# Kernel tuning notes

Hardware: AMD Instinct MI355X
Metric: run time of the kernel (lower is better)

## Reference

```python
import jax, jax.numpy as jnp
import numpy as np

GAMMA = 10.0          # entropy_regularizer_weight
N_ITERS = 10          # optimization_steps
EPS = np.float32(7.0 / 3 - 4.0 / 3 - 1.0)  # matches tf.constant(7/3-4/3-1, float32)

B, W, H, D = 128, 28, 28, 512
S = 128               # support_size


def setup_inputs() -> dict:
    key = jax.random.key(0)
    k1, k2 = jax.random.split(key)
    features = jax.random.normal(k1, (B, W, H, D), dtype=jnp.float32)
    # GlorotUniform-like init for the target support (learned codebook)
    limit = np.sqrt(6.0 / (S + D)).astype(np.float32)
    target_support = jax.random.uniform(k2, (S, D), dtype=jnp.float32,
                                        minval=-limit, maxval=limit)
    return {"features": features, "target_support": target_support}


def _l2norm(x):
    return x / jnp.sqrt(jnp.sum(x * x, axis=-1, keepdims=True))


def reference(features, target_support):
    b, w, h, d = features.shape
    s = target_support.shape[0]
    n = w * h  # num_feats

    t = _l2norm(target_support)                 # (S, D)
    f = _l2norm(features).reshape(b, n, d)      # (B, N, D)

    # pairwise squared L2 distance between normalized vectors: 2 - 2*cos
    c = 2.0 - 2.0 * jnp.einsum('sd,bnd->bsn', t, f)  # (B, S, N)

    K = jnp.exp(-GAMMA * c)                     # (B, S, N)
    q = jnp.full((1, 1, n), 1.0 / n, dtype=jnp.float32)  # marginal over feats
    p = jnp.full((1, 1, s), 1.0 / s, dtype=jnp.float32)  # marginal over support

    u = jnp.ones((b, 1, s), dtype=jnp.float32)
    Kt = jnp.swapaxes(K, 1, 2)                  # (B, N, S)
    for _ in range(N_ITERS):
        v = q / (jnp.matmul(u, K) + EPS)        # (B, 1, N)
        u = p / (jnp.matmul(v, Kt) + EPS)       # (B, 1, S)
    v = q / (jnp.matmul(u, K) + EPS)

    # transport plan Pi = u^T * K * v  -> (B, S, N)
    Pi = jnp.swapaxes(u, 1, 2) * K * v
    return Pi
```

## Files before the change

kernel.cpp:

```cpp
#include <hip/hip_runtime.h>
#include <hip/hip_fp16.h>

#define EPS_C   2.2204460492503131e-16f
#define NS      128
#define ND      512
#define NN      784
#define NB      128
#define BSN     (NS*NN)
#define QM      (1.0f/784.0f)
#define LOG2E20 28.853900817779268f

typedef __attribute__((ext_vector_type(8))) short bf16x8;
typedef __attribute__((ext_vector_type(4))) float f32x4;

static __device__ __forceinline__ ushort f2bf(float x) {
    uint u = __float_as_uint(x);
    uint r = (u + 0x7FFFu + ((u >> 16) & 1u)) >> 16;
    return (ushort)r;
}
static __device__ __forceinline__ float bf2f(ushort h) {
    return __uint_as_float(((uint)h) << 16);
}

__global__ __launch_bounds__(128)
void tnorm_kernel(const float* __restrict__ t,
                  ushort* __restrict__ tnh, ushort* __restrict__ tnl) {
    int s = blockIdx.x, tid = threadIdx.x;
    float4 x = ((const float4*)(t + s * ND))[tid];
    float ss = x.x*x.x + x.y*x.y + x.z*x.z + x.w*x.w;
#pragma unroll
    for (int off = 1; off < 64; off <<= 1) ss += __shfl_xor(ss, off);
    __shared__ float red[2];
    if ((tid & 63) == 0) red[tid >> 6] = ss;
    __syncthreads();
    float rs = 1.0f / sqrtf(red[0] + red[1]);
    float y[4] = {x.x*rs, x.y*rs, x.z*rs, x.w*rs};
    ushort h[4], l[4];
#pragma unroll
    for (int k = 0; k < 4; k++) {
        h[k] = f2bf(y[k]);
        l[k] = f2bf(y[k] - bf2f(h[k]));
    }
    *(ushort4*)(tnh + s * ND + tid * 4) = make_ushort4(h[0], h[1], h[2], h[3]);
    *(ushort4*)(tnl + s * ND + tid * 4) = make_ushort4(l[0], l[1], l[2], l[3]);
}

#define LDK 40

__global__ void __launch_bounds__(256)
__attribute__((amdgpu_waves_per_eu(2, 2)))
gemm_k_kernel(const ushort* __restrict__ Ahi, const ushort* __restrict__ Alo,
              const float* __restrict__ f, uint* __restrict__ Kp) {
    __shared__ ushort Ash[2][NS * LDK];
    __shared__ ushort Bsh[2][NS * LDK];
    __shared__ float  ssq_sh[128];

    const int tid  = threadIdx.x;
    const int lane = tid & 63;
    const int wid  = tid >> 6;
    const int wm   = wid & 1;
    const int wn   = wid >> 1;
    const int j0   = blockIdx.x * 128;

    const int arow  = tid & 127;
    const int ahalf = tid >> 7;
    const int brow  = tid >> 3;
    const int bcol4 = (tid & 7) * 4;

    const ushort* Asrc = (ahalf ? Alo : Ahi) + (size_t)arow * ND;
    const float* bPtr[4];
#pragma unroll
    for (int p = 0; p < 4; p++)
        bPtr[p] = f + (size_t)(j0 + p * 32 + brow) * ND + bcol4;

    f32x4 acc[4][4];
#pragma unroll
    for (int i = 0; i < 4; i++)
#pragma unroll
        for (int j = 0; j < 4; j++) acc[i][j] = (f32x4){0.f, 0.f, 0.f, 0.f};
    float ssqp[4] = {0.f, 0.f, 0.f, 0.f};

    const int mrow = lane & 15;
    const int koff = (lane >> 4) * 8;

    uint4 aReg[4];
    float4 bReg[4];
    {
        const uint4* ap = (const uint4*)Asrc;
        aReg[0] = ap[0]; aReg[1] = ap[1]; aReg[2] = ap[2]; aReg[3] = ap[3];
#pragma unroll
        for (int p = 0; p < 4; p++) bReg[p] = *(const float4*)bPtr[p];
    }

    for (int d0 = 0; d0 < ND; d0 += 32) {
        {
            ushort* dst = &Ash[ahalf][arow * LDK];
            *(uint4*)(dst)      = aReg[0];
            *(uint4*)(dst + 8)  = aReg[1];
            *(uint4*)(dst + 16) = aReg[2];
            *(uint4*)(dst + 24) = aReg[3];
        }
#pragma unroll
        for (int p = 0; p < 4; p++) {
            float4 v = bReg[p];
            ssqp[p] += v.x*v.x + v.y*v.y + v.z*v.z + v.w*v.w;
            ushort h0 = f2bf(v.x), h1 = f2bf(v.y), h2 = f2bf(v.z), h3 = f2bf(v.w);
            ushort l0 = f2bf(v.x - bf2f(h0)), l1 = f2bf(v.y - bf2f(h1));
            ushort l2 = f2bf(v.z - bf2f(h2)), l3 = f2bf(v.w - bf2f(h3));
            int c = p * 32 + brow;
            *(uint2*)&Bsh[0][c * LDK + bcol4] =
                make_uint2((uint)h0 | ((uint)h1 << 16), (uint)h2 | ((uint)h3 << 16));
            *(uint2*)&Bsh[1][c * LDK + bcol4] =
                make_uint2((uint)l0 | ((uint)l1 << 16), (uint)l2 | ((uint)l3 << 16));
        }
        __syncthreads();
        if (d0 + 32 < ND) {
            const uint4* ap = (const uint4*)(Asrc + d0 + 32);
            aReg[0] = ap[0]; aReg[1] = ap[1]; aReg[2] = ap[2]; aReg[3] = ap[3];
#pragma unroll
            for (int p = 0; p < 4; p++)
                bReg[p] = *(const float4*)(bPtr[p] + d0 + 32);
        }
        bf16x8 ah[4], bb[4];
#pragma unroll
        for (int i = 0; i < 4; i++)
            ah[i] = *(const bf16x8*)&Ash[0][(wm*64 + i*16 + mrow) * LDK + koff];
#pragma unroll
        for (int j = 0; j < 4; j++)
            bb[j] = *(const bf16x8*)&Bsh[0][(wn*64 + j*16 + mrow) * LDK + koff];
#pragma unroll
        for (int i = 0; i < 4; i++)
#pragma unroll
            for (int j = 0; j < 4; j++)
                acc[i][j] = __builtin_amdgcn_mfma_f32_16x16x32_bf16(ah[i], bb[j], acc[i][j], 0, 0, 0);
        {
            bf16x8 al[4];
#pragma unroll
            for (int i = 0; i < 4; i++)
                al[i] = *(const bf16x8*)&Ash[1][(wm*64 + i*16 + mrow) * LDK + koff];
#pragma unroll
            for (int i = 0; i < 4; i++)
#pragma unroll
                for (int j = 0; j < 4; j++)
                    acc[i][j] = __builtin_amdgcn_mfma_f32_16x16x32_bf16(al[i], bb[j], acc[i][j], 0, 0, 0);
        }
#pragma unroll
        for (int j = 0; j < 4; j++)
            bb[j] = *(const bf16x8*)&Bsh[1][(wn*64 + j*16 + mrow) * LDK + koff];
#pragma unroll
        for (int i = 0; i < 4; i++)
#pragma unroll
            for (int j = 0; j < 4; j++)
                acc[i][j] = __builtin_amdgcn_mfma_f32_16x16x32_bf16(ah[i], bb[j], acc[i][j], 0, 0, 0);
        __syncthreads();
    }

#pragma unroll
    for (int p = 0; p < 4; p++) {
#pragma unroll
        for (int off = 1; off < 8; off <<= 1) ssqp[p] += __shfl_xor(ssqp[p], off);
    }
    if ((tid & 7) == 0) {
#pragma unroll
        for (int p = 0; p < 4; p++) ssq_sh[p * 32 + (tid >> 3)] = ssqp[p];
    }
    __syncthreads();

    const int quad4 = (lane >> 4) << 2;
#pragma unroll
    for (int jt = 0; jt < 4; jt++) {
        int cloc = wn * 64 + jt * 16 + mrow;
        float rq = rsqrtf(ssq_sh[cloc]) * LOG2E20;
        int jg = j0 + cloc;
        int b2 = jg / NN;
        int nn = jg - b2 * NN;
        int jj = nn >> 6, l = nn & 63;
#pragma unroll
        for (int i = 0; i < 4; i++) {
            int s0 = wm * 64 + i * 16 + quad4;
            float k0 = exp2f(acc[i][jt][0] * rq);
            float k1 = exp2f(acc[i][jt][1] * rq);
            float k2v = exp2f(acc[i][jt][2] * rq);
            float k3 = exp2f(acc[i][jt][3] * rq);
            __half2 lo = __halves2half2(__float2half(k0), __float2half(k1));
            __half2 hi = __halves2half2(__float2half(k2v), __float2half(k3));
            size_t dw = (((size_t)(b2 * 16 + (s0 >> 3)) * 13 + jj) * 64 + l) * 4
                        + ((s0 & 7) >> 1);
            *(uint2*)(Kp + dw) = make_uint2(__builtin_bit_cast(uint, lo),
                                            __builtin_bit_cast(uint, hi));
        }
    }
}

#define VSCALE 64.0f
#define PM64   (VSCALE/128.0f)
#define EPS64  (EPS_C*VSCALE)

__global__ void __launch_bounds__(1024)
__attribute__((amdgpu_waves_per_eu(4, 4)))
sinkhorn_kernel(const uint* __restrict__ Kp, float* __restrict__ Pi) {
    __shared__ float slab[16 * NN];
    __shared__ float v_sh[NN];
    const int b    = blockIdx.x;
    const int tid  = threadIdx.x;
    const int lane = tid & 63;
    const int w    = tid >> 6;
    float* Pib = Pi + (size_t)b * BSN;

    const uint4* kbase = (const uint4*)Kp + (size_t)(b * 16 + w) * 13 * 64 + lane;
    __half2 k2[13][4];
#pragma unroll
    for (int j = 0; j < 13; j++) {
        uint4 t = kbase[j * 64];
        k2[j][0] = __builtin_bit_cast(__half2, t.x);
        k2[j][1] = __builtin_bit_cast(__half2, t.y);
        k2[j][2] = __builtin_bit_cast(__half2, t.z);
        k2[j][3] = __builtin_bit_cast(__half2, t.w);
    }
    if (lane >= 16) {
#pragma unroll
        for (int rp = 0; rp < 4; rp++) k2[12][rp] = __halves2half2(__half(0.f), __half(0.f));
    }

    __half2 u2[4];
    float uf[8];
#pragma unroll
    for (int rp = 0; rp < 4; rp++) u2[rp] = __halves2half2(__half(1.f), __half(1.f));
#pragma unroll
    for (int r = 0; r < 8; r++) uf[r] = 1.f;

    float* myrow = &slab[w * NN];

    for (int it = 0; it <= 10; ++it) {
#pragma unroll
        for (int j = 0; j < 13; j++) {
            int n = lane + (j << 6);
            float pa = 0.f;
#pragma unroll
            for (int rp = 0; rp < 4; rp++)
                pa = __builtin_amdgcn_fdot2(k2[j][rp], u2[rp], pa, false);
            if (n < NN) myrow[n] = pa;
        }
        __syncthreads();
        if (tid < NN) {
            float s0 = 0.f, s1 = 0.f, s2 = 0.f, s3 = 0.f;
#pragma unroll
            for (int w2 = 0; w2 < 16; w2 += 4) {
                s0 += slab[(w2 + 0) * NN + tid];
                s1 += slab[(w2 + 1) * NN + tid];
                s2 += slab[(w2 + 2) * NN + tid];
                s3 += slab[(w2 + 3) * NN + tid];
            }
            v_sh[tid] = QM / (((s0 + s1) + (s2 + s3)) + EPS_C);
        }
        __syncthreads();
        if (it == 10) break;
        __half2 acc2[4];
#pragma unroll
        for (int rp = 0; rp < 4; rp++) acc2[rp] = __halves2half2(__half(0.f), __half(0.f));
#pragma unroll
        for (int j = 0; j < 13; j++) {
            int n = lane + (j << 6);
            int ni = (n < NN) ? n : 0;
            float vv = v_sh[ni] * VSCALE;
            __half vh = __float2half(vv);
            __half2 vh2 = __halves2half2(vh, vh);
#pragma unroll
            for (int rp = 0; rp < 4; rp++)
                acc2[rp] = __hfma2(vh2, k2[j][rp], acc2[rp]);
        }
#pragma unroll
        for (int rp = 0; rp < 4; rp++) {
#pragma unroll
            for (int off = 1; off < 64; off <<= 1) {
                int y = __shfl_xor(__builtin_bit_cast(int, acc2[rp]), off);
                acc2[rp] = __hadd2(acc2[rp], __builtin_bit_cast(__half2, y));
            }
            float2 af = __half22float2(acc2[rp]);
            uf[2*rp]     = PM64 / (af.x + EPS64);
            uf[2*rp + 1] = PM64 / (af.y + EPS64);
            u2[rp] = __halves2half2(__float2half(uf[2*rp]), __float2half(uf[2*rp+1]));
        }
    }

#pragma unroll
    for (int j = 0; j < 13; j++) {
        int n = lane + (j << 6);
        if (n < NN) {
            float vv = v_sh[n];
#pragma unroll
            for (int rp = 0; rp < 4; rp++) {
                float2 kk = __half22float2(k2[j][rp]);
                Pib[(size_t)(8*w + 2*rp    ) * NN + n] = uf[2*rp]     * kk.x * vv;
                Pib[(size_t)(8*w + 2*rp + 1) * NN + n] = uf[2*rp + 1] * kk.y * vv;
            }
        }
    }
}

extern "C" void kernel_launch(void* const* d_in, const int* in_sizes, int n_in,
                              void* d_out, int out_size, void* d_ws, size_t ws_size,
                              hipStream_t stream) {
    const float* feat = (const float*)d_in[0];
    const float* tsup = (const float*)d_in[1];
    float* out = (float*)d_out;

    ushort* tnh = (ushort*)d_ws;
    ushort* tnl = tnh + NS * ND;
    uint*   Kp  = (uint*)(tnl + NS * ND);

    tnorm_kernel<<<NS, 128, 0, stream>>>(tsup, tnh, tnl);
    gemm_k_kernel<<<(NB * NN) / 128, 256, 0, stream>>>(tnh, tnl, feat, Kp);
    sinkhorn_kernel<<<NB, 1024, 0, stream>>>(Kp, out);
}
```

Baseline: 366.5 us.

## Load A fragments directly from global, use packed bf16 convert, relax occupancy

The GEMM kernel no longer stages the normalized support (hi/lo bf16 split) through shared memory. Each wave now loads its MFMA A fragments straight from global memory (L2-resident, 128x512), which removes half the LDS traffic and footprint. The hi/lo bf16 split of the features now uses the hardware v_cvt_pk_bf16_f32 instruction instead of manual rounding. waves_per_eu is widened to allow more occupancy. The catch is that A loads are no longer prefetched a tile ahead, so global latency may be exposed just before the MFMAs. Redundant A reads across the wn waves also rely on cache.

```diff
diff --git a/kernel.cpp b/kernel.cpp
--- a/kernel.cpp
+++ b/kernel.cpp
@@ -21,6 +21,11 @@
 static __device__ __forceinline__ float bf2f(ushort h) {
     return __uint_as_float(((uint)h) << 16);
 }
+static __device__ __forceinline__ uint cvtpk_bf16(float a, float b) {
+    uint r;
+    asm("v_cvt_pk_bf16_f32 %0, %1, %2" : "=v"(r) : "v"(a), "v"(b));
+    return r;
+}
 
 __global__ __launch_bounds__(128)
 void tnorm_kernel(const float* __restrict__ t,
@@ -48,10 +53,9 @@
 #define LDK 40
 
 __global__ void __launch_bounds__(256)
-__attribute__((amdgpu_waves_per_eu(2, 2)))
+__attribute__((amdgpu_waves_per_eu(2, 4)))
 gemm_k_kernel(const ushort* __restrict__ Ahi, const ushort* __restrict__ Alo,
               const float* __restrict__ f, uint* __restrict__ Kp) {
-    __shared__ ushort Ash[2][NS * LDK];
     __shared__ ushort Bsh[2][NS * LDK];
     __shared__ float  ssq_sh[128];
 
@@ -62,17 +66,26 @@
     const int wn   = wid >> 1;
     const int j0   = blockIdx.x * 128;
 
-    const int arow  = tid & 127;
-    const int ahalf = tid >> 7;
     const int brow  = tid >> 3;
     const int bcol4 = (tid & 7) * 4;
 
-    const ushort* Asrc = (ahalf ? Alo : Ahi) + (size_t)arow * ND;
     const float* bPtr[4];
 #pragma unroll
     for (int p = 0; p < 4; p++)
         bPtr[p] = f + (size_t)(j0 + p * 32 + brow) * ND + bcol4;
 
+    const int mrow = lane & 15;
+    const int koff = (lane >> 4) * 8;
+
+    const ushort* aPtrH[4];
+    const ushort* aPtrL[4];
+#pragma unroll
+    for (int i = 0; i < 4; i++) {
+        int r = wm * 64 + i * 16 + mrow;
+        aPtrH[i] = Ahi + (size_t)r * ND + koff;
+        aPtrL[i] = Alo + (size_t)r * ND + koff;
+    }
+
     f32x4 acc[4][4];
 #pragma unroll
     for (int i = 0; i < 4; i++)
@@ -80,51 +93,40 @@
         for (int j = 0; j < 4; j++) acc[i][j] = (f32x4){0.f, 0.f, 0.f, 0.f};
     float ssqp[4] = {0.f, 0.f, 0.f, 0.f};
 
-    const int mrow = lane & 15;
-    const int koff = (lane >> 4) * 8;
-
-    uint4 aReg[4];
     float4 bReg[4];
-    {
-        const uint4* ap = (const uint4*)Asrc;
-        aReg[0] = ap[0]; aReg[1] = ap[1]; aReg[2] = ap[2]; aReg[3] = ap[3];
-#pragma unroll
-        for (int p = 0; p < 4; p++) bReg[p] = *(const float4*)bPtr[p];
-    }
+#pragma unroll
+    for (int p = 0; p < 4; p++) bReg[p] = *(const float4*)bPtr[p];
 
     for (int d0 = 0; d0 < ND; d0 += 32) {
-        {
-            ushort* dst = &Ash[ahalf][arow * LDK];
-            *(uint4*)(dst)      = aReg[0];
-            *(uint4*)(dst + 8)  = aReg[1];
-            *(uint4*)(dst + 16) = aReg[2];
-            *(uint4*)(dst + 24) = aReg[3];
-        }
+        bf16x8 ah[4], al[4];
+#pragma unroll
+        for (int i = 0; i < 4; i++) ah[i] = *(const bf16x8*)(aPtrH[i] + d0);
+#pragma unroll
+        for (int i = 0; i < 4; i++) al[i] = *(const bf16x8*)(aPtrL[i] + d0);
+
 #pragma unroll
         for (int p = 0; p < 4; p++) {
             float4 v = bReg[p];
             ssqp[p] += v.x*v.x + v.y*v.y + v.z*v.z + v.w*v.w;
-            ushort h0 = f2bf(v.x), h1 = f2bf(v.y), h2 = f2bf(v.z), h3 = f2bf(v.w);
-            ushort l0 = f2bf(v.x - bf2f(h0)), l1 = f2bf(v.y - bf2f(h1));
-            ushort l2 = f2bf(v.z - bf2f(h2)), l3 = f2bf(v.w - bf2f(h3));
+            uint hA = cvtpk_bf16(v.x, v.y);
+            uint hB = cvtpk_bf16(v.z, v.w);
+            float rx = v.x - __uint_as_float(hA << 16);
+            float ry = v.y - __uint_as_float(hA & 0xFFFF0000u);
+            float rz = v.z - __uint_as_float(hB << 16);
+            float rw = v.w - __uint_as_float(hB & 0xFFFF0000u);
+            uint lA = cvtpk_bf16(rx, ry);
+            uint lB = cvtpk_bf16(rz, rw);
             int c = p * 32 + brow;
-            *(uint2*)&Bsh[0][c * LDK + bcol4] =
-                make_uint2((uint)h0 | ((uint)h1 << 16), (uint)h2 | ((uint)h3 << 16));
-            *(uint2*)&Bsh[1][c * LDK + bcol4] =
-                make_uint2((uint)l0 | ((uint)l1 << 16), (uint)l2 | ((uint)l3 << 16));
+            *(uint2*)&Bsh[0][c * LDK + bcol4] = make_uint2(hA, hB);
+            *(uint2*)&Bsh[1][c * LDK + bcol4] = make_uint2(lA, lB);
         }
         __syncthreads();
         if (d0 + 32 < ND) {
-            const uint4* ap = (const uint4*)(Asrc + d0 + 32);
-            aReg[0] = ap[0]; aReg[1] = ap[1]; aReg[2] = ap[2]; aReg[3] = ap[3];
 #pragma unroll
             for (int p = 0; p < 4; p++)
                 bReg[p] = *(const float4*)(bPtr[p] + d0 + 32);
         }
-        bf16x8 ah[4], bb[4];
-#pragma unroll
-        for (int i = 0; i < 4; i++)
-            ah[i] = *(const bf16x8*)&Ash[0][(wm*64 + i*16 + mrow) * LDK + koff];
+        bf16x8 bb[4];
 #pragma unroll
         for (int j = 0; j < 4; j++)
             bb[j] = *(const bf16x8*)&Bsh[0][(wn*64 + j*16 + mrow) * LDK + koff];
@@ -133,17 +135,11 @@
 #pragma unroll
             for (int j = 0; j < 4; j++)
                 acc[i][j] = __builtin_amdgcn_mfma_f32_16x16x32_bf16(ah[i], bb[j], acc[i][j], 0, 0, 0);
-        {
-            bf16x8 al[4];
-#pragma unroll
-            for (int i = 0; i < 4; i++)
-                al[i] = *(const bf16x8*)&Ash[1][(wm*64 + i*16 + mrow) * LDK + koff];
-#pragma unroll
-            for (int i = 0; i < 4; i++)
-#pragma unroll
-                for (int j = 0; j < 4; j++)
-                    acc[i][j] = __builtin_amdgcn_mfma_f32_16x16x32_bf16(al[i], bb[j], acc[i][j], 0, 0, 0);
-        }
+#pragma unroll
+        for (int i = 0; i < 4; i++)
+#pragma unroll
+            for (int j = 0; j < 4; j++)
+                acc[i][j] = __builtin_amdgcn_mfma_f32_16x16x32_bf16(al[i], bb[j], acc[i][j], 0, 0, 0);
 #pragma unroll
         for (int j = 0; j < 4; j++)
             bb[j] = *(const bf16x8*)&Bsh[1][(wn*64 + j*16 + mrow) * LDK + koff];
```

Result: faster. 357.1 us (-2.6%).
